# Performance work log

Measured on AMD Instinct MI355X. Metric: run time of the kernel, lower is better.

## Reference

```python
import jax, jax.numpy as jnp
import numpy as np

N_NODES = 500_000
N_OUTDIM = 256
HIDDEN = 512
N_REPRE = 128
NUM_GRAPHS = 1024  # = max(graph_idx) + 1 by construction


def setup_inputs() -> dict:
    key = jax.random.key(0)
    ks = jax.random.split(key, 8)
    node_states = jax.random.normal(ks[0], (N_NODES, N_OUTDIM), dtype=jnp.float32)
    graph_idx = jnp.sort(jax.random.randint(ks[1], (N_NODES,), 0, NUM_GRAPHS, dtype=jnp.int64))
    s1 = 1.0 / np.sqrt(N_OUTDIM)
    s2 = 1.0 / np.sqrt(HIDDEN)
    W1 = jax.random.uniform(ks[2], (N_OUTDIM, HIDDEN), jnp.float32, -s1, s1)
    b1 = jax.random.uniform(ks[3], (HIDDEN,), jnp.float32, -s1, s1)
    W2 = jax.random.uniform(ks[4], (HIDDEN, HIDDEN), jnp.float32, -s2, s2)
    b2 = jax.random.uniform(ks[5], (HIDDEN,), jnp.float32, -s2, s2)
    W3 = jax.random.uniform(ks[6], (HIDDEN, N_REPRE), jnp.float32, -s2, s2)
    b3 = jax.random.uniform(ks[7], (N_REPRE,), jnp.float32, -s2, s2)
    return {"node_states": node_states, "graph_idx": graph_idx,
            "W1": W1, "b1": b1, "W2": W2, "b2": b2, "W3": W3, "b3": b3}


def reference(node_states, graph_idx, W1, b1, W2, b2, W3, b3):
    # 3-layer MLP: Linear -> ReLU -> Linear -> ReLU -> Linear
    h = jax.nn.relu(node_states @ W1 + b1)          # [N, HIDDEN]
    h = jax.nn.relu(h @ W2 + b2)                     # [N, HIDDEN]
    y = h @ W3 + b3                                  # [N, N_REPRE]
    # gated = sigmoid(y) * y  (SiLU)
    g = jax.nn.sigmoid(y) * y
    # scatter-add per-graph segment sum -> [NUM_GRAPHS, N_REPRE]
    return jax.ops.segment_sum(g, graph_idx, num_segments=NUM_GRAPHS)
```

## Files before the change

kernel.cpp:

```cpp
#include <hip/hip_runtime.h>
#include <stdint.h>


typedef short bf16x8 __attribute__((ext_vector_type(8)));
typedef float f32x4  __attribute__((ext_vector_type(4)));

#define N_NODES   500000
#define BM        32
#define N_BLOCKS  (N_NODES / BM)
#define N_GRAPHS  1024
#define N_OUT     128

#define W1P_ELEMS (256*512)
#define W2P_ELEMS (512*512)
#define W3P_ELEMS (512*128)
#define W2P_OFF   (W1P_ELEMS)
#define W3P_OFF   (W1P_ELEMS + W2P_ELEMS)
#define PREPACK_THREADS ((W1P_ELEMS + W2P_ELEMS + W3P_ELEMS) / 8)

__device__ __forceinline__ short f2bf(float x) {
    uint32_t u = __float_as_uint(x);
    u += 0x7fffu + ((u >> 16) & 1u);
    return (short)(u >> 16);
}

__global__ void prepack_weights(const float* __restrict__ W1,
                                const float* __restrict__ W2,
                                const float* __restrict__ W3,
                                short* __restrict__ wp) {
    int tid = blockIdx.x * blockDim.x + threadIdx.x;
    if (tid >= PREPACK_THREADS) return;
    const float* src; int N, kmask, kshift, dstoff, local;
    if (tid < 16384) {
        src = W1; N = 512; kmask = 7;  kshift = 3; dstoff = 0;       local = tid;
    } else if (tid < 49152) {
        src = W2; N = 512; kmask = 15; kshift = 4; dstoff = W2P_OFF; local = tid - 16384;
    } else {
        src = W3; N = 128; kmask = 15; kshift = 4; dstoff = W3P_OFF; local = tid - 49152;
    }
    const int lane = local & 63;
    const int tile = local >> 6;
    const int kt = tile & kmask;
    const int nt = tile >> kshift;
    const int k0 = kt * 32 + (lane >> 4) * 8;
    const int n  = nt * 16 + (lane & 15);
    const float* s = src + (size_t)k0 * N + n;
    union { bf16x8 v; short e[8]; } u;
#pragma unroll
    for (int j = 0; j < 8; ++j) u.e[j] = f2bf(s[(size_t)j * N]);
    *((bf16x8*)(wp + dstoff) + local) = u.v;
}

__launch_bounds__(256, 2)
__global__ void fused_mlp(const float* __restrict__ X,
                          const int*   __restrict__ gidx,
                          const short* __restrict__ wp,
                          const float* __restrict__ b1,
                          const float* __restrict__ b2,
                          const float* __restrict__ b3,
                          float* __restrict__ out) {
    __shared__ __align__(16) char lds[65536];
    char* R0 = lds;
    char* R1 = lds + 32768;

    const int t    = threadIdx.x;
    const int lane = t & 63;
    const int wave = t >> 6;
    const int q    = lane >> 4;
    const int l15  = lane & 15;
    const int64_t rowBase = (int64_t)blockIdx.x * BM;

    const f32x4 zero4 = {0.f, 0.f, 0.f, 0.f};

    {
        const int m  = t >> 3;
        const int s  = t & 7;
        const int sw = m & 7;
        const float* xr = X + (rowBase + m) * 256;
#pragma unroll
        for (int i = 0; i < 8; ++i) {
            const int col = (s + 8 * i) * 4;
            const float4 f = *(const float4*)(xr + col);
            short4 h;
            h.x = f2bf(f.x); h.y = f2bf(f.y); h.z = f2bf(f.z); h.w = f2bf(f.w);
            const int c = col >> 3;
            const int off = m * 512 + ((c ^ sw) << 4) + ((col >> 2) & 1) * 8;
            *(short4*)(R0 + off) = h;
        }
    }
    __syncthreads();

    {
        f32x4 acc[2][8];
#pragma unroll
        for (int rt = 0; rt < 2; ++rt)
#pragma unroll
            for (int c8 = 0; c8 < 8; ++c8) acc[rt][c8] = zero4;
        const bf16x8* wB = (const bf16x8*)wp;
        for (int kt = 0; kt < 8; ++kt) {
            bf16x8 a[2];
#pragma unroll
            for (int rt = 0; rt < 2; ++rt) {
                const int m = rt * 16 + l15;
                const int c = kt * 4 + q;
                a[rt] = *(const bf16x8*)(R0 + m * 512 + ((c ^ (m & 7)) << 4));
            }
#pragma unroll
            for (int c8 = 0; c8 < 8; ++c8) {
                const int ct = wave * 8 + c8;
                const bf16x8 b = wB[(ct * 8 + kt) * 64 + lane];
                acc[0][c8] = __builtin_amdgcn_mfma_f32_16x16x32_bf16(a[0], b, acc[0][c8], 0, 0, 0);
                acc[1][c8] = __builtin_amdgcn_mfma_f32_16x16x32_bf16(a[1], b, acc[1][c8], 0, 0, 0);
            }
        }
#pragma unroll
        for (int c8 = 0; c8 < 8; ++c8) {
            const int n = (wave * 8 + c8) * 16 + l15;
            const float bias = b1[n];
            const int cg = n >> 3;
            const int nl = n & 7;
#pragma unroll
            for (int rt = 0; rt < 2; ++rt)
#pragma unroll
                for (int r = 0; r < 4; ++r) {
                    const int m = rt * 16 + q * 4 + r;
                    float v = acc[rt][c8][r] + bias;
                    v = fmaxf(v, 0.f);
                    *(short*)(R1 + m * 1024 + ((cg ^ (m & 7)) << 4) + nl * 2) = f2bf(v);
                }
        }
    }
    __syncthreads();

    {
        f32x4 acc[2][8];
#pragma unroll
        for (int rt = 0; rt < 2; ++rt)
#pragma unroll
            for (int c8 = 0; c8 < 8; ++c8) acc[rt][c8] = zero4;
        const bf16x8* wB = (const bf16x8*)wp + (W2P_OFF >> 3);
        for (int kt = 0; kt < 16; ++kt) {
            bf16x8 a[2];
#pragma unroll
            for (int rt = 0; rt < 2; ++rt) {
                const int m = rt * 16 + l15;
                const int c = kt * 4 + q;
                a[rt] = *(const bf16x8*)(R1 + m * 1024 + ((c ^ (m & 7)) << 4));
            }
#pragma unroll
            for (int c8 = 0; c8 < 8; ++c8) {
                const int ct = wave * 8 + c8;
                const bf16x8 b = wB[(ct * 16 + kt) * 64 + lane];
                acc[0][c8] = __builtin_amdgcn_mfma_f32_16x16x32_bf16(a[0], b, acc[0][c8], 0, 0, 0);
                acc[1][c8] = __builtin_amdgcn_mfma_f32_16x16x32_bf16(a[1], b, acc[1][c8], 0, 0, 0);
            }
        }
#pragma unroll
        for (int c8 = 0; c8 < 8; ++c8) {
            const int n = (wave * 8 + c8) * 16 + l15;
            const float bias = b2[n];
            const int cg = n >> 3;
            const int nl = n & 7;
#pragma unroll
            for (int rt = 0; rt < 2; ++rt)
#pragma unroll
                for (int r = 0; r < 4; ++r) {
                    const int m = rt * 16 + q * 4 + r;
                    float v = acc[rt][c8][r] + bias;
                    v = fmaxf(v, 0.f);
                    *(short*)(R0 + m * 1024 + ((cg ^ (m & 7)) << 4) + nl * 2) = f2bf(v);
                }
        }
    }
    __syncthreads();

    {
        f32x4 acc[2][2];
#pragma unroll
        for (int rt = 0; rt < 2; ++rt)
#pragma unroll
            for (int c2 = 0; c2 < 2; ++c2) acc[rt][c2] = zero4;
        const bf16x8* wB = (const bf16x8*)wp + (W3P_OFF >> 3);
        for (int kt = 0; kt < 16; ++kt) {
            bf16x8 a[2];
#pragma unroll
            for (int rt = 0; rt < 2; ++rt) {
                const int m = rt * 16 + l15;
                const int c = kt * 4 + q;
                a[rt] = *(const bf16x8*)(R0 + m * 1024 + ((c ^ (m & 7)) << 4));
            }
#pragma unroll
            for (int c2 = 0; c2 < 2; ++c2) {
                const int ct = wave * 2 + c2;
                const bf16x8 b = wB[(ct * 16 + kt) * 64 + lane];
                acc[0][c2] = __builtin_amdgcn_mfma_f32_16x16x32_bf16(a[0], b, acc[0][c2], 0, 0, 0);
                acc[1][c2] = __builtin_amdgcn_mfma_f32_16x16x32_bf16(a[1], b, acc[1][c2], 0, 0, 0);
            }
        }
        float* yl = (float*)R1;
#pragma unroll
        for (int c2 = 0; c2 < 2; ++c2) {
            const int n = (wave * 2 + c2) * 16 + l15;
            const float bias = b3[n];
#pragma unroll
            for (int rt = 0; rt < 2; ++rt)
#pragma unroll
                for (int r = 0; r < 4; ++r) {
                    const int m = rt * 16 + q * 4 + r;
                    const float yv = acc[rt][c2][r] + bias;
                    const float gv = yv / (1.f + __expf(-yv));
                    yl[m * 132 + n] = gv;
                }
        }
    }
    __syncthreads();

    {
        int* gs = (int*)R0;
        if (t < BM) gs[t] = gidx[rowBase + t];
        __syncthreads();
        const int col = t & 127;
        const int r0  = (t >> 7) * 16;
        const float* yl = (const float*)R1;
        int   gprev = gs[r0];
        float acc   = 0.f;
        for (int r = r0; r < r0 + 16; ++r) {
            const int gr = gs[r];
            if (gr != gprev) {
                atomicAdd(out + gprev * N_OUT + col, acc);
                acc = 0.f;
                gprev = gr;
            }
            acc += yl[r * 132 + col];
        }
        atomicAdd(out + gprev * N_OUT + col, acc);
    }
}

extern "C" void kernel_launch(void* const* d_in, const int* in_sizes, int n_in,
                              void* d_out, int out_size, void* d_ws, size_t ws_size,
                              hipStream_t stream) {
    const float* X    = (const float*)d_in[0];
    const int*   gidx = (const int*)  d_in[1];
    const float* W1   = (const float*)d_in[2];
    const float* b1   = (const float*)d_in[3];
    const float* W2   = (const float*)d_in[4];
    const float* b2   = (const float*)d_in[5];
    const float* W3   = (const float*)d_in[6];
    const float* b3   = (const float*)d_in[7];
    float* out = (float*)d_out;
    short* wp  = (short*)d_ws;

    hipMemsetAsync(d_out, 0, sizeof(float) * N_GRAPHS * N_OUT, stream);

    prepack_weights<<<PREPACK_THREADS / 256, 256, 0, stream>>>(W1, W2, W3, wp);

    fused_mlp<<<N_BLOCKS, 256, 0, stream>>>(X, gidx, wp, b1, b2, b3, out);
}
```

Baseline: 1.192 ms.

## Enlarge row tile to 128 with 8 waves for higher weight reuse

Each block now handles 128 rows with 512 threads. Each wave computes 8 row tiles by 4 column tiles, so every weight fragment fetched from global memory feeds 8 MFMAs instead of 2. The input is staged into LDS in two K halves, and a single 128 KB hidden buffer is reused in place across layers, using about 160 KB of dynamic LDS. A tail guard handles the last partial block. The trade-off is likely one block per CU because of the LDS size, plus heavy accumulator register pressure that could cause spills.

Result: slower. 2.054 ms (+72.3%).

```diff
diff --git a/kernel.cpp b/kernel.cpp
--- a/kernel.cpp
+++ b/kernel.cpp
@@ -6,10 +6,13 @@
 typedef float f32x4  __attribute__((ext_vector_type(4)));
 
 #define N_NODES   500000
-#define BM        32
-#define N_BLOCKS  (N_NODES / BM)
+#define BM        128
+#define N_BLOCKS  ((N_NODES + BM - 1) / BM)
 #define N_GRAPHS  1024
 #define N_OUT     128
+
+#define HX_BYTES  131072
+#define LDS_BYTES (HX_BYTES + 32768)
 
 #define W1P_ELEMS (256*512)
 #define W2P_ELEMS (512*512)
@@ -23,6 +26,7 @@
     u += 0x7fffu + ((u >> 16) & 1u);
     return (short)(u >> 16);
 }
+__device__ __forceinline__ int swz(int m) { return (m ^ (m >> 3)) & 7; }
 
 __global__ void prepack_weights(const float* __restrict__ W1,
                                 const float* __restrict__ W2,
@@ -51,7 +55,7 @@
     *((bf16x8*)(wp + dstoff) + local) = u.v;
 }
 
-__launch_bounds__(256, 2)
+__launch_bounds__(512, 2)
 __global__ void fused_mlp(const float* __restrict__ X,
                           const int*   __restrict__ gidx,
                           const short* __restrict__ wp,
@@ -59,9 +63,9 @@
                           const float* __restrict__ b2,
                           const float* __restrict__ b3,
                           float* __restrict__ out) {
-    __shared__ __align__(16) char lds[65536];
-    char* R0 = lds;
-    char* R1 = lds + 32768;
+    extern __shared__ char lds[];
+    char* HX = lds;
+    char* XS = lds + HX_BYTES;
 
     const int t    = threadIdx.x;
     const int lane = t & 63;
@@ -69,171 +73,169 @@
     const int q    = lane >> 4;
     const int l15  = lane & 15;
     const int64_t rowBase = (int64_t)blockIdx.x * BM;
+    const int valid = (int)min((int64_t)BM, (int64_t)N_NODES - rowBase);
 
     const f32x4 zero4 = {0.f, 0.f, 0.f, 0.f};
-
+    f32x4 acc[8][4];
+
+#pragma unroll
+    for (int rt = 0; rt < 8; ++rt)
+#pragma unroll
+        for (int c = 0; c < 4; ++c) acc[rt][c] = zero4;
+
+    const bf16x8* w1 = (const bf16x8*)wp;
+    for (int half = 0; half < 2; ++half) {
+        if (half) __syncthreads();
+        {
+            int m  = t >> 5;
+            const int ch = t & 31;
+            const int g   = ch >> 1;
+            const int sel = ch & 1;
+#pragma unroll
+            for (int p = 0; p < 8; ++p, m += 16) {
+                float4 f = {0.f, 0.f, 0.f, 0.f};
+                if (m < valid)
+                    f = *(const float4*)(X + (rowBase + m) * 256 + half * 128 + ch * 4);
+                short4 h4;
+                h4.x = f2bf(f.x); h4.y = f2bf(f.y); h4.z = f2bf(f.z); h4.w = f2bf(f.w);
+                *(short4*)(XS + m * 256 + ((g ^ swz(m)) << 4) + sel * 8) = h4;
+            }
+        }
+        __syncthreads();
+        for (int ktl = 0; ktl < 4; ++ktl) {
+            bf16x8 a[8];
+#pragma unroll
+            for (int rt = 0; rt < 8; ++rt) {
+                const int m = rt * 16 + l15;
+                const int g = ktl * 4 + q;
+                a[rt] = *(const bf16x8*)(XS + m * 256 + ((g ^ swz(m)) << 4));
+            }
+#pragma unroll
+            for (int c = 0; c < 4; ++c) {
+                const int nt = wave * 4 + c;
+                const bf16x8 b = w1[(nt * 8 + half * 4 + ktl) * 64 + lane];
+#pragma unroll
+                for (int rt = 0; rt < 8; ++rt)
+                    acc[rt][c] = __builtin_amdgcn_mfma_f32_16x16x32_bf16(a[rt], b, acc[rt][c], 0, 0, 0);
+            }
+        }
+    }
+#pragma unroll
+    for (int c = 0; c < 4; ++c) {
+        const int n = (wave * 4 + c) * 16 + l15;
+        const float bias = b1[n];
+        const int cg = n >> 3;
+        const int nl = n & 7;
+#pragma unroll
+        for (int rt = 0; rt < 8; ++rt)
+#pragma unroll
+            for (int r = 0; r < 4; ++r) {
+                const int m = rt * 16 + q * 4 + r;
+                float v = acc[rt][c][r] + bias;
+                v = fmaxf(v, 0.f);
+                *(short*)(HX + m * 1024 + ((cg ^ swz(m)) << 4) + nl * 2) = f2bf(v);
+            }
+    }
+    __syncthreads();
+
+#pragma unroll
+    for (int rt = 0; rt < 8; ++rt)
+#pragma unroll
+        for (int c = 0; c < 4; ++c) acc[rt][c] = zero4;
+
+    const bf16x8* w2 = (const bf16x8*)wp + (W2P_OFF >> 3);
+    for (int kt = 0; kt < 16; ++kt) {
+        bf16x8 a[8];
+#pragma unroll
+        for (int rt = 0; rt < 8; ++rt) {
+            const int m = rt * 16 + l15;
+            const int g = kt * 4 + q;
+            a[rt] = *(const bf16x8*)(HX + m * 1024 + ((g ^ swz(m)) << 4));
+        }
+#pragma unroll
+        for (int c = 0; c < 4; ++c) {
+            const int nt = wave * 4 + c;
+            const bf16x8 b = w2[(nt * 16 + kt) * 64 + lane];
+#pragma unroll
+            for (int rt = 0; rt < 8; ++rt)
+                acc[rt][c] = __builtin_amdgcn_mfma_f32_16x16x32_bf16(a[rt], b, acc[rt][c], 0, 0, 0);
+        }
+    }
+    __syncthreads();
+#pragma unroll
+    for (int c = 0; c < 4; ++c) {
+        const int n = (wave * 4 + c) * 16 + l15;
+        const float bias = b2[n];
+        const int cg = n >> 3;
+        const int nl = n & 7;
+#pragma unroll
+        for (int rt = 0; rt < 8; ++rt)
+#pragma unroll
+            for (int r = 0; r < 4; ++r) {
+                const int m = rt * 16 + q * 4 + r;
+                float v = acc[rt][c][r] + bias;
+                v = fmaxf(v, 0.f);
+                *(short*)(HX + m * 1024 + ((cg ^ swz(m)) << 4) + nl * 2) = f2bf(v);
+            }
+    }
+    __syncthreads();
+
+    f32x4 acc3[8];
+#pragma unroll
+    for (int rt = 0; rt < 8; ++rt) acc3[rt] = zero4;
+
+    const bf16x8* w3 = (const bf16x8*)wp + (W3P_OFF >> 3);
+    for (int kt = 0; kt < 16; ++kt) {
+        bf16x8 a[8];
+#pragma unroll
+        for (int rt = 0; rt < 8; ++rt) {
+            const int m = rt * 16 + l15;
+            const int g = kt * 4 + q;
+            a[rt] = *(const bf16x8*)(HX + m * 1024 + ((g ^ swz(m)) << 4));
+        }
+        const bf16x8 b = w3[(wave * 16 + kt) * 64 + lane];
+#pragma unroll
+        for (int rt = 0; rt < 8; ++rt)
+            acc3[rt] = __builtin_amdgcn_mfma_f32_16x16x32_bf16(a[rt], b, acc3[rt], 0, 0, 0);
+    }
+    __syncthreads();
     {
-        const int m  = t >> 3;
-        const int s  = t & 7;
-        const int sw = m & 7;
-        const float* xr = X + (rowBase + m) * 256;
-#pragma unroll
-        for (int i = 0; i < 8; ++i) {
-            const int col = (s + 8 * i) * 4;
-            const float4 f = *(const float4*)(xr + col);
-            short4 h;
-            h.x = f2bf(f.x); h.y = f2bf(f.y); h.z = f2bf(f.z); h.w = f2bf(f.w);
-            const int c = col >> 3;
-            const int off = m * 512 + ((c ^ sw) << 4) + ((col >> 2) & 1) * 8;
-            *(short4*)(R0 + off) = h;
-        }
+        float* yl = (float*)HX;
+        const int n = wave * 16 + l15;
+        const float bias = b3[n];
+#pragma unroll
+        for (int rt = 0; rt < 8; ++rt)
+#pragma unroll
+            for (int r = 0; r < 4; ++r) {
+                const int m = rt * 16 + q * 4 + r;
+                const float yv = acc3[rt][r] + bias;
+                yl[m * 132 + n] = yv / (1.f + __expf(-yv));
+            }
+        int* gs = (int*)XS;
+        if (t < BM) gs[t] = (t < valid) ? gidx[rowBase + t] : 0;
     }
     __syncthreads();
 
     {
-        f32x4 acc[2][8];
-#pragma unroll
-        for (int rt = 0; rt < 2; ++rt)
-#pragma unroll
-            for (int c8 = 0; c8 < 8; ++c8) acc[rt][c8] = zero4;
-        const bf16x8* wB = (const bf16x8*)wp;
-        for (int kt = 0; kt < 8; ++kt) {
-            bf16x8 a[2];
-#pragma unroll
-            for (int rt = 0; rt < 2; ++rt) {
-                const int m = rt * 16 + l15;
-                const int c = kt * 4 + q;
-                a[rt] = *(const bf16x8*)(R0 + m * 512 + ((c ^ (m & 7)) << 4));
-            }
-#pragma unroll
-            for (int c8 = 0; c8 < 8; ++c8) {
-                const int ct = wave * 8 + c8;
-                const bf16x8 b = wB[(ct * 8 + kt) * 64 + lane];
-                acc[0][c8] = __builtin_amdgcn_mfma_f32_16x16x32_bf16(a[0], b, acc[0][c8], 0, 0, 0);
-                acc[1][c8] = __builtin_amdgcn_mfma_f32_16x16x32_bf16(a[1], b, acc[1][c8], 0, 0, 0);
-            }
-        }
-#pragma unroll
-        for (int c8 = 0; c8 < 8; ++c8) {
-            const int n = (wave * 8 + c8) * 16 + l15;
-            const float bias = b1[n];
-            const int cg = n >> 3;
-            const int nl = n & 7;
-#pragma unroll
-            for (int rt = 0; rt < 2; ++rt)
-#pragma unroll
-                for (int r = 0; r < 4; ++r) {
-                    const int m = rt * 16 + q * 4 + r;
-                    float v = acc[rt][c8][r] + bias;
-                    v = fmaxf(v, 0.f);
-                    *(short*)(R1 + m * 1024 + ((cg ^ (m & 7)) << 4) + nl * 2) = f2bf(v);
+        const int col = t & 127;
+        const int r0  = (t >> 7) * 32;
+        const int r1  = min(r0 + 32, valid);
+        if (r0 < valid) {
+            const int*   gs = (const int*)XS;
+            const float* yl = (const float*)HX;
+            int   gprev = gs[r0];
+            float s     = 0.f;
+            for (int r = r0; r < r1; ++r) {
+                const int g = gs[r];
+                if (g != gprev) {
+                    atomicAdd(out + gprev * N_OUT + col, s);
+                    s = 0.f;
+                    gprev = g;
                 }
-        }
-    }
-    __syncthreads();
-
-    {
-        f32x4 acc[2][8];
-#pragma unroll
-        for (int rt = 0; rt < 2; ++rt)
-#pragma unroll
-            for (int c8 = 0; c8 < 8; ++c8) acc[rt][c8] = zero4;
-        const bf16x8* wB = (const bf16x8*)wp + (W2P_OFF >> 3);
-        for (int kt = 0; kt < 16; ++kt) {
-            bf16x8 a[2];
-#pragma unroll
-            for (int rt = 0; rt < 2; ++rt) {
-                const int m = rt * 16 + l15;
-                const int c = kt * 4 + q;
-                a[rt] = *(const bf16x8*)(R1 + m * 1024 + ((c ^ (m & 7)) << 4));
-            }
-#pragma unroll
-            for (int c8 = 0; c8 < 8; ++c8) {
-                const int ct = wave * 8 + c8;
-                const bf16x8 b = wB[(ct * 16 + kt) * 64 + lane];
-                acc[0][c8] = __builtin_amdgcn_mfma_f32_16x16x32_bf16(a[0], b, acc[0][c8], 0, 0, 0);
-                acc[1][c8] = __builtin_amdgcn_mfma_f32_16x16x32_bf16(a[1], b, acc[1][c8], 0, 0, 0);
-            }
-        }
-#pragma unroll
-        for (int c8 = 0; c8 < 8; ++c8) {
-            const int n = (wave * 8 + c8) * 16 + l15;
-            const float bias = b2[n];
-            const int cg = n >> 3;
-            const int nl = n & 7;
-#pragma unroll
-            for (int rt = 0; rt < 2; ++rt)
-#pragma unroll
-                for (int r = 0; r < 4; ++r) {
-                    const int m = rt * 16 + q * 4 + r;
-                    float v = acc[rt][c8][r] + bias;
-                    v = fmaxf(v, 0.f);
-                    *(short*)(R0 + m * 1024 + ((cg ^ (m & 7)) << 4) + nl * 2) = f2bf(v);
-                }
-        }
-    }
-    __syncthreads();
-
-    {
-        f32x4 acc[2][2];
-#pragma unroll
-        for (int rt = 0; rt < 2; ++rt)
-#pragma unroll
-            for (int c2 = 0; c2 < 2; ++c2) acc[rt][c2] = zero4;
-        const bf16x8* wB = (const bf16x8*)wp + (W3P_OFF >> 3);
-        for (int kt = 0; kt < 16; ++kt) {
-            bf16x8 a[2];
-#pragma unroll
-            for (int rt = 0; rt < 2; ++rt) {
-                const int m = rt * 16 + l15;
-                const int c = kt * 4 + q;
-                a[rt] = *(const bf16x8*)(R0 + m * 1024 + ((c ^ (m & 7)) << 4));
-            }
-#pragma unroll
-            for (int c2 = 0; c2 < 2; ++c2) {
-                const int ct = wave * 2 + c2;
-                const bf16x8 b = wB[(ct * 16 + kt) * 64 + lane];
-                acc[0][c2] = __builtin_amdgcn_mfma_f32_16x16x32_bf16(a[0], b, acc[0][c2], 0, 0, 0);
-                acc[1][c2] = __builtin_amdgcn_mfma_f32_16x16x32_bf16(a[1], b, acc[1][c2], 0, 0, 0);
-            }
-        }
-        float* yl = (float*)R1;
-#pragma unroll
-        for (int c2 = 0; c2 < 2; ++c2) {
-            const int n = (wave * 2 + c2) * 16 + l15;
-            const float bias = b3[n];
-#pragma unroll
-            for (int rt = 0; rt < 2; ++rt)
-#pragma unroll
-                for (int r = 0; r < 4; ++r) {
-                    const int m = rt * 16 + q * 4 + r;
-                    const float yv = acc[rt][c2][r] + bias;
-                    const float gv = yv / (1.f + __expf(-yv));
-                    yl[m * 132 + n] = gv;
-                }
-        }
-    }
-    __syncthreads();
-
-    {
-        int* gs = (int*)R0;
-        if (t < BM) gs[t] = gidx[rowBase + t];
-        __syncthreads();
-        const int col = t & 127;
-        const int r0  = (t >> 7) * 16;
-        const float* yl = (const float*)R1;
-        int   gprev = gs[r0];
-        float acc   = 0.f;
-        for (int r = r0; r < r0 + 16; ++r) {
-            const int gr = gs[r];
-            if (gr != gprev) {
-                atomicAdd(out + gprev * N_OUT + col, acc);
-                acc = 0.f;
-                gprev = gr;
-            }
-            acc += yl[r * 132 + col];
-        }
-        atomicAdd(out + gprev * N_OUT + col, acc);
+                s += yl[r * 132 + col];
+            }
+            atomicAdd(out + gprev * N_OUT + col, s);
+        }
     }
 }
 
@@ -251,9 +253,12 @@
     float* out = (float*)d_out;
     short* wp  = (short*)d_ws;
 
+    hipFuncSetAttribute((const void*)fused_mlp,
+                        hipFuncAttributeMaxDynamicSharedMemorySize, LDS_BYTES);
+
     hipMemsetAsync(d_out, 0, sizeof(float) * N_GRAPHS * N_OUT, stream);
 
     prepack_weights<<<PREPACK_THREADS / 256, 256, 0, stream>>>(W1, W2, W3, wp);
 
-    fused_mlp<<<N_BLOCKS, 256, 0, stream>>>(X, gidx, wp, b1, b2, b3, out);
-}
+    fused_mlp<<<N_BLOCKS, 512, LDS_BYTES, stream>>>(X, gidx, wp, b1, b2, b3, out);
+}
```
